# Kernel tuning notes

Hardware: AMD Instinct MI355X
Metric: run time of the kernel (lower is better)

Reference implementation:

```python
import jax, jax.numpy as jnp
import numpy as np

N_FFT = 200; HOP = 100; N_FREQ = N_FFT // 2 + 1  # 101
EMB = 256; HEADS = 8; DHEAD = EMB // HEADS; DEPTH = 4
N_CH = 23; B = 256; TS = 2000
MASK_RATIO = 0.9


def _layernorm(x, s, b):
    mu = jnp.mean(x, -1, keepdims=True)
    var = jnp.mean((x - mu) ** 2, -1, keepdims=True)
    return (x - mu) * jax.lax.rsqrt(var + 1e-5) * s + b


def _posenc(T, d):
    pos = jnp.arange(T, dtype=jnp.float32)[:, None]
    div = jnp.exp(jnp.arange(0, d, 2, dtype=jnp.float32) * (-np.log(10000.0) / d))
    pe = jnp.zeros((T, d), jnp.float32)
    pe = pe.at[:, 0::2].set(jnp.sin(pos * div))
    pe = pe.at[:, 1::2].set(jnp.cos(pos * div))
    return pe


def setup_inputs() -> dict:
    key = jax.random.key(0)
    ks = jax.random.split(key, 12)
    def n(k, shape):
        return (jax.random.normal(k, shape) * 0.02).astype(jnp.float32)
    T = 1 + (TS - N_FFT) // HOP  # 19
    S = N_CH * T                 # 437
    return dict(
        x=jax.random.normal(ks[0], (B, N_CH, TS), jnp.float32),
        mask_noise=jax.random.uniform(ks[1], (B, S, EMB), dtype=jnp.float32),
        W_proj=n(ks[2], (N_FREQ, EMB)), b_proj=jnp.zeros((EMB,), jnp.float32),
        channel_tokens=n(ks[3], (N_CH, EMB)),
        ln1_s=jnp.ones((DEPTH, EMB), jnp.float32), ln1_b=jnp.zeros((DEPTH, EMB), jnp.float32),
        Wq=n(ks[4], (DEPTH, EMB, EMB)), Wk=n(ks[5], (DEPTH, EMB, EMB)),
        Wv=n(ks[6], (DEPTH, EMB, EMB)), Wo=n(ks[7], (DEPTH, EMB, EMB)),
        bo=jnp.zeros((DEPTH, EMB), jnp.float32),
        ln2_s=jnp.ones((DEPTH, EMB), jnp.float32), ln2_b=jnp.zeros((DEPTH, EMB), jnp.float32),
        W1=n(ks[8], (DEPTH, EMB, 4 * EMB)), b1=jnp.zeros((DEPTH, 4 * EMB), jnp.float32),
        W2=n(ks[9], (DEPTH, 4 * EMB, EMB)), b2=jnp.zeros((DEPTH, EMB), jnp.float32),
    )


def _forward(x, mask_noise, W_proj, b_proj, channel_tokens,
             ln1_s, ln1_b, Wq, Wk, Wv, Wo, bo, ln2_s, ln2_b, W1, b1, W2, b2):
    Bb, C, ts = x.shape
    T = 1 + (ts - N_FFT) // HOP
    # ---- vectorized per-channel STFT (rect window, center=False, onesided) ----
    idx = jnp.arange(T)[:, None] * HOP + jnp.arange(N_FFT)[None, :]  # [T, n_fft]
    frames = x[:, :, idx]                                            # [B,C,T,n_fft]
    spec = jnp.abs(jnp.fft.rfft(frames, axis=-1)).astype(x.dtype)    # [B,C,T,F]
    # patch embedding (Linear over freq), channel token, positional encoding
    emb = spec @ W_proj + b_proj                                     # [B,C,T,E]
    emb = emb + channel_tokens[:C][None, :, None, :]
    emb = emb + _posenc(T, emb.shape[-1])[None, None]
    emb = emb.reshape(Bb, C * T, -1)                                 # [B,S,E]
    # ---- random masking (mask_ratio=0.9 as hard-coded in forward) ----
    mask = mask_noise < MASK_RATIO
    masked = jnp.where(mask, jnp.zeros((), emb.dtype), emb)
    # ---- LinearAttentionTransformer (non-causal linear attention, pre-norm) ----
    h = masked
    for l in range(DEPTH):
        y = _layernorm(h, ln1_s[l], ln1_b[l])
        S = y.shape[1]
        q = (y @ Wq[l]).reshape(Bb, S, HEADS, DHEAD).transpose(0, 2, 1, 3)
        k = (y @ Wk[l]).reshape(Bb, S, HEADS, DHEAD).transpose(0, 2, 1, 3)
        v = (y @ Wv[l]).reshape(Bb, S, HEADS, DHEAD).transpose(0, 2, 1, 3)
        q = jax.nn.softmax(q, axis=-1) * (DHEAD ** -0.5)
        k = jax.nn.softmax(k, axis=2)  # softmax over sequence
        ctx = jnp.einsum('bhnd,bhne->bhde', k, v)     # [B,H,d,d] global context
        att = jnp.einsum('bhnd,bhde->bhne', q, ctx)   # [B,H,S,d]
        att = att.transpose(0, 2, 1, 3).reshape(Bb, S, EMB)
        h = h + att @ Wo[l] + bo[l]
        y = _layernorm(h, ln2_s[l], ln2_b[l])
        h = h + jax.nn.gelu(y @ W1[l] + b1[l]) @ W2[l] + b2[l]
    return emb, masked, h, mask


def reference(x, mask_noise, W_proj, b_proj, channel_tokens,
              ln1_s, ln1_b, Wq, Wk, Wv, Wo, bo, ln2_s, ln2_b, W1, b1, W2, b2):
    return _forward(x, mask_noise, W_proj, b_proj, channel_tokens,
                    ln1_s, ln1_b, Wq, Wk, Wv, Wo, bo, ln2_s, ln2_b, W1, b1, W2, b2)
```

## Files before the change

kernel.cpp:

```cpp
#include <hip/hip_runtime.h>

#define BB    256
#define NCH   23
#define TT    19
#define SS    437
#define BSR   111872
#define EMBD  256
#define NHEAD 8
#define DH    32
#define NFREQ 101
#define NFFT  200
#define HOPSZ 100
#define TSLEN 2000
#define HID   1024
#define NDEPTH 4
#define NTOK  28639232
#define QKVW  768
#define WL    786432
#define CDL   3584

typedef __attribute__((ext_vector_type(8))) __bf16 bf16x8;
typedef __attribute__((ext_vector_type(8))) unsigned short u16x8;
typedef __attribute__((ext_vector_type(4))) float  f32x4;

__device__ __forceinline__ float gelu_f(float x){
    return 0.5f*x*(1.0f + tanhf(0.7978845608028654f*(x + 0.044715f*x*x*x)));
}
__device__ __forceinline__ unsigned short f2b(float f){
    unsigned u = __float_as_uint(f);
    return (unsigned short)((u + 0x7FFFu + ((u >> 16) & 1u)) >> 16);
}
__device__ __forceinline__ float b2f(unsigned short h){
    return __uint_as_float(((unsigned)h) << 16);
}

__device__ __forceinline__ void swz_tile(int& bx, int& by){
    int nx = gridDim.x, nwg = nx * gridDim.y;
    int lid = blockIdx.y * nx + blockIdx.x;
    int q = nwg >> 3, r = nwg & 7;
    int xcd = lid & 7, off = lid >> 3;
    int wgid = (xcd < r ? xcd*(q+1) : r*(q+1) + (xcd-r)*q) + off;
    bx = wgid % nx; by = wgid / nx;
}

__global__ void init_twb(unsigned short* __restrict__ tw){
    int i = blockIdx.x*256 + threadIdx.x;
    if(i >= 256*256) return;
    int n = i >> 8, k = i & 255;
    float v = 0.f;
    if(k < NFFT && n < 2*NFREQ){
        int f = n >> 1;
        int ph = (f * k) % NFFT;
        float ang = 6.283185307179586f * (float)ph / (float)NFFT;
        v = (n & 1) ? sinf(ang) : cosf(ang);
    }
    tw[i] = f2b(v);
}

__global__ void init_pe(float* __restrict__ pe){
    int i = blockIdx.x*256 + threadIdx.x;
    if(i >= TT*EMBD) return;
    int t = i / EMBD, e = i % EMBD;
    int j = e >> 1;
    float div = expf((float)(2*j) * (-9.210340371976184f/256.0f));
    float ang = (float)t * div;
    pe[i] = (e & 1) ? cosf(ang) : sinf(ang);
}

__global__ void wprep_proj(const float* __restrict__ Wp, unsigned short* __restrict__ Wt){
    int i = blockIdx.x*256 + threadIdx.x;
    if(i >= 256*128) return;
    int e = i >> 7, k = i & 127;
    Wt[i] = f2b(k < NFREQ ? Wp[(size_t)k*EMBD + e] : 0.f);
}

__global__ void wprep_qkv(const float* __restrict__ Wq, const float* __restrict__ Wk,
                          const float* __restrict__ Wv, const float* __restrict__ ln1s,
                          unsigned short* __restrict__ wbuf){
    long i = (long)blockIdx.x*256 + threadIdx.x;
    if(i >= (long)NDEPTH*QKVW*EMBD) return;
    int l = (int)(i / (QKVW*EMBD));
    int rem = (int)(i % (QKVW*EMBD));
    int n = rem >> 8, k = rem & 255;
    const float* W = (n < 256) ? Wq : (n < 512) ? Wk : Wv;
    float s = ln1s[l*EMBD + k];
    wbuf[(size_t)l*WL + rem] = f2b(s * W[(size_t)l*65536 + (size_t)k*256 + (n & 255)]);
}
__global__ void wprep_wo(const float* __restrict__ Wo, unsigned short* __restrict__ wbuf){
    int i = blockIdx.x*256 + threadIdx.x;
    if(i >= NDEPTH*65536) return;
    int l = i >> 16, rem = i & 65535;
    int n = rem >> 8, k = rem & 255;
    wbuf[(size_t)l*WL + 196608 + rem] = f2b(Wo[(size_t)l*65536 + (size_t)k*256 + n]);
}
__global__ void wprep_w1(const float* __restrict__ W1, const float* __restrict__ ln2s,
                         unsigned short* __restrict__ wbuf){
    long i = (long)blockIdx.x*256 + threadIdx.x;
    if(i >= (long)NDEPTH*262144) return;
    int l = (int)(i >> 18), rem = (int)(i & 262143);
    int n = rem >> 8, k = rem & 255;
    float s = ln2s[l*EMBD + k];
    wbuf[(size_t)l*WL + 262144 + rem] = f2b(s * W1[(size_t)l*262144 + (size_t)k*1024 + n]);
}
__global__ void wprep_w2(const float* __restrict__ W2, unsigned short* __restrict__ wbuf){
    long i = (long)blockIdx.x*256 + threadIdx.x;
    if(i >= (long)NDEPTH*262144) return;
    int l = (int)(i >> 18), rem = (int)(i & 262143);
    int n = rem >> 10, k = rem & 1023;
    wbuf[(size_t)l*WL + 524288 + rem] = f2b(W2[(size_t)l*262144 + (size_t)k*256 + n]);
}

__global__ void prep_cd(const float* __restrict__ Wq, const float* __restrict__ Wk,
                        const float* __restrict__ Wv, const float* __restrict__ W1,
                        const float* __restrict__ ln1s, const float* __restrict__ ln1b,
                        const float* __restrict__ ln2s, const float* __restrict__ ln2b,
                        const float* __restrict__ b1, float* __restrict__ cd){
    int i = blockIdx.x*256 + threadIdx.x;
    if(i >= NDEPTH*1792) return;
    int l = i / 1792, r = i % 1792;
    float c = 0.f, d = 0.f;
    if(r < 768){
        const float* W = (r < 256) ? Wq : (r < 512) ? Wk : Wv;
        int n = r & 255;
        for(int k = 0; k < 256; ++k){
            float w = W[(size_t)l*65536 + (size_t)k*256 + n];
            c = fmaf(ln1s[l*EMBD+k], w, c);
            d = fmaf(ln1b[l*EMBD+k], w, d);
        }
        cd[(size_t)l*CDL + r]       = c;
        cd[(size_t)l*CDL + 768 + r] = d;
    } else {
        int n = r - 768;
        for(int k = 0; k < 256; ++k){
            float w = W1[(size_t)l*262144 + (size_t)k*1024 + n];
            c = fmaf(ln2s[l*EMBD+k], w, c);
            d = fmaf(ln2b[l*EMBD+k], w, d);
        }
        cd[(size_t)l*CDL + 1536 + n] = c;
        cd[(size_t)l*CDL + 2560 + n] = d + b1[l*HID + n];
    }
}

#define GEMM_CORE(A_, B_, K_) \
    f32x4 acc[4][4]; \
    _Pragma("unroll") \
    for(int i=0;i<4;++i) \
        _Pragma("unroll") \
        for(int jj=0;jj<4;++jj) acc[i][jj] = (f32x4){0.f,0.f,0.f,0.f}; \
    const int srow0 = w*32 + (l>>3); \
    const int sgrp  = l & 7; \
    for(int k0 = 0; k0 < (K_); k0 += 64){ \
        _Pragma("unroll") \
        for(int it=0; it<4; ++it){ \
            int row  = srow0 + it*8; \
            int colA = ((sgrp ^ (row & 7)) << 3); \
            const unsigned short* ga = (A_) + (size_t)(m0+row)*(K_) + k0 + colA; \
            const unsigned short* gb = (B_) + (size_t)(n0+row)*(K_) + k0 + colA; \
            __builtin_amdgcn_global_load_lds( \
                (__attribute__((address_space(1))) void*)ga, \
                (__attribute__((address_space(3))) void*)(As + w*2048 + it*512), \
                16, 0, 0); \
            __builtin_amdgcn_global_load_lds( \
                (__attribute__((address_space(1))) void*)gb, \
                (__attribute__((address_space(3))) void*)(Bs + w*2048 + it*512), \
                16, 0, 0); \
        } \
        __syncthreads(); \
        GEMM_MFMA_PHASE \
        __syncthreads(); \
    }

#define GEMM_MFMA_PHASE \
        _Pragma("unroll") \
        for(int kk=0; kk<2; ++kk){ \
            bf16x8 af[4], bfr[4]; \
            _Pragma("unroll") \
            for(int mi=0;mi<4;++mi){ \
                int row = wr*64 + mi*16 + (l & 15); \
                int grp = kk*4 + (l >> 4); \
                af[mi] = *(const bf16x8*)&As[row*64 + ((grp ^ (row&7))<<3)]; \
            } \
            _Pragma("unroll") \
            for(int ni=0;ni<4;++ni){ \
                int row = wc*64 + ni*16 + (l & 15); \
                int grp = kk*4 + (l >> 4); \
                bfr[ni] = *(const bf16x8*)&Bs[row*64 + ((grp ^ (row&7))<<3)]; \
            } \
            _Pragma("unroll") \
            for(int mi=0;mi<4;++mi) \
                _Pragma("unroll") \
                for(int ni=0;ni<4;++ni) \
                    acc[mi][ni] = __builtin_amdgcn_mfma_f32_16x16x32_bf16( \
                        af[mi], bfr[ni], acc[mi][ni], 0, 0, 0); \
        }

#define STATS_REDUCE_STORE(rb_, s1_, s2_) \
    { \
        _Pragma("unroll") \
        for(int o=1;o<16;o<<=1){ s1_ += __shfl_xor(s1_, o, 64); s2_ += __shfl_xor(s2_, o, 64); } \
        if(cn == 0){ \
            slds[((rb_)*2 + wc)*2 + 0] = s1_; \
            slds[((rb_)*2 + wc)*2 + 1] = s2_; \
        } \
    }

template<int MODE, int STATS>
__global__ __launch_bounds__(256, 4) void gemm_mfma(
    const unsigned short* __restrict__ A, const unsigned short* __restrict__ Bt,
    const float* __restrict__ bias, void* __restrict__ Cv,
    const unsigned short* __restrict__ Cin, float* __restrict__ sums,
    int M, int N, int K)
{
    __shared__ __align__(16) unsigned short As[128*64];
    __shared__ __align__(16) unsigned short Bs[128*64];
    const int tid = threadIdx.x;
    const int w = tid >> 6, l = tid & 63;
    int bx, by; swz_tile(bx, by);
    const int m0 = by * 128, n0 = bx * 128;
    const int wr = w >> 1, wc = w & 1;
    GEMM_CORE(A, Bt, K)
    const int cn  = l & 15;
    const int cr4 = (l >> 4) * 4;
    float* slds = (float*)As;
    float bnv[4];
    #pragma unroll
    for(int ni=0;ni<4;++ni) bnv[ni] = bias[n0 + wc*64 + ni*16 + cn];
    #pragma unroll
    for(int mi=0;mi<4;++mi){
        #pragma unroll
        for(int r=0;r<4;++r){
            int rb = wr*64 + mi*16 + cr4 + r;
            int m  = m0 + rb;
            float s1 = 0.f, s2 = 0.f;
            #pragma unroll
            for(int ni=0;ni<4;++ni){
                int n = n0 + wc*64 + ni*16 + cn;
                size_t off = (size_t)m*N + n;
                float v = b2f(Cin[off]) + acc[mi][ni][r] + bnv[ni];
                if(MODE == 1) ((unsigned short*)Cv)[off] = f2b(v);
                else          ((float*)Cv)[off] = v;
                if(STATS){ s1 += v; s2 += v*v; }
            }
            if(STATS) STATS_REDUCE_STORE(rb, s1, s2)
        }
    }
    if(STATS){
        __syncthreads();
        if(tid < 128){
            float t1 = slds[(tid*2+0)*2+0] + slds[(tid*2+1)*2+0];
            float t2 = slds[(tid*2+0)*2+1] + slds[(tid*2+1)*2+1];
            atomicAdd(&sums[(size_t)(m0+tid)*2],   t1);
            atomicAdd(&sums[(size_t)(m0+tid)*2+1], t2);
        }
    }
}

template<int GELU>
__global__ __launch_bounds__(256, 4) void gemm_ln(
    const unsigned short* __restrict__ A, const unsigned short* __restrict__ Bt,
    void* __restrict__ Cv, const float* __restrict__ sums,
    const float* __restrict__ cvec, const float* __restrict__ dvec,
    int M, int N, int K)
{
    __shared__ __align__(16) unsigned short As[128*64];
    __shared__ __align__(16) unsigned short Bs[128*64];
    const int tid = threadIdx.x;
    const int w = tid >> 6, l = tid & 63;
    int bx, by; swz_tile(bx, by);
    const int m0 = by * 128, n0 = bx * 128;
    const int wr = w >> 1, wc = w & 1;
    GEMM_CORE(A, Bt, K)
    const int cn  = l & 15;
    const int cr4 = (l >> 4) * 4;
    float cv[4], dv[4];
    #pragma unroll
    for(int ni=0;ni<4;++ni){
        int n = n0 + wc*64 + ni*16 + cn;
        cv[ni] = cvec[n]; dv[ni] = dvec[n];
    }
    #pragma unroll
    for(int mi=0;mi<4;++mi){
        #pragma unroll
        for(int r=0;r<4;++r){
            int m = m0 + wr*64 + mi*16 + cr4 + r;
            float mu  = sums[(size_t)m*2]   * (1.0f/256.0f);
            float ex2 = sums[(size_t)m*2+1] * (1.0f/256.0f);
            float rs = rsqrtf(ex2 - mu*mu + 1e-5f);
            float c0 = rs * mu;
            #pragma unroll
            for(int ni=0;ni<4;++ni){
                int n = n0 + wc*64 + ni*16 + cn;
                float y = rs*acc[mi][ni][r] - c0*cv[ni] + dv[ni];
                ((unsigned short*)Cv)[(size_t)m*N + n] = f2b(GELU ? gelu_f(y) : y);
            }
        }
    }
}

__global__ __launch_bounds__(256) void gemm_dft(
    const float* __restrict__ x, const unsigned short* __restrict__ Bt,
    unsigned short* __restrict__ spec)
{
    const int K = 256;
    __shared__ __align__(16) unsigned short As[128*64];
    __shared__ __align__(16) unsigned short Bs[128*64];
    const int tid = threadIdx.x;
    const int w = tid >> 6, l = tid & 63;
    int bx, by; swz_tile(bx, by);
    const int m0 = by * 128, n0 = bx * 128;
    const int wr = w >> 1, wc = w & 1;
    f32x4 acc[4][4];
    #pragma unroll
    for(int i=0;i<4;++i)
        #pragma unroll
        for(int jj=0;jj<4;++jj) acc[i][jj] = (f32x4){0.f,0.f,0.f,0.f};
    const int sgrp = l & 7;
    for(int k0 = 0; k0 < K; k0 += 64){
        #pragma unroll
        for(int it=0; it<4; ++it){
            int row = w*32 + it*8 + (l>>3);
            int kg  = sgrp ^ (row & 7);
            int kb  = k0 + kg*8;
            int m   = m0 + row;
            int t   = m % TT;
            long bc = m / TT;
            const float* src = x + bc*(long)TSLEN + (long)t*HOPSZ + kb;
            u16x8 v;
            #pragma unroll
            for(int j=0;j<8;++j){
                float f = (kb + j < NFFT) ? src[j] : 0.f;
                v[j] = f2b(f);
            }
            *(u16x8*)&As[row*64 + sgrp*8] = v;
            int colB = (kg << 3);
            const unsigned short* gb = Bt + (size_t)(n0+row)*K + k0 + colB;
            __builtin_amdgcn_global_load_lds(
                (__attribute__((address_space(1))) void*)gb,
                (__attribute__((address_space(3))) void*)(Bs + w*2048 + it*512),
                16, 0, 0);
        }
        __syncthreads();
        GEMM_MFMA_PHASE
        __syncthreads();
    }
    const int cn  = l & 15;
    const int cr4 = (l >> 4) * 4;
    #pragma unroll
    for(int ni=0;ni<4;++ni){
        int n = n0 + wc*64 + ni*16 + cn;
        #pragma unroll
        for(int mi=0;mi<4;++mi){
            int mB = m0 + wr*64 + mi*16 + cr4;
            #pragma unroll
            for(int r=0;r<4;++r){
                float own = acc[mi][ni][r];
                float par = __shfl_xor(own, 1, 64);
                if(!(cn & 1)){
                    float sv = sqrtf(own*own + par*par);
                    spec[(size_t)(mB+r)*128 + (n >> 1)] = f2b(sv);
                }
            }
        }
    }
}

__global__ __launch_bounds__(256) void gemm_emb(
    const unsigned short* __restrict__ A, const unsigned short* __restrict__ Bt,
    const float* __restrict__ bp, const float* __restrict__ ctok,
    const float* __restrict__ pe, const float* __restrict__ noise,
    float* __restrict__ o_emb, float* __restrict__ o_masked,
    float* __restrict__ o_mask, unsigned short* __restrict__ bufH,
    float* __restrict__ sums)
{
    const int K = 128, N = 256;
    __shared__ __align__(16) unsigned short As[128*64];
    __shared__ __align__(16) unsigned short Bs[128*64];
    const int tid = threadIdx.x;
    const int w = tid >> 6, l = tid & 63;
    int bx, by; swz_tile(bx, by);
    const int m0 = by * 128, n0 = bx * 128;
    const int wr = w >> 1, wc = w & 1;
    GEMM_CORE(A, Bt, K)
    const int cn  = l & 15;
    const int cr4 = (l >> 4) * 4;
    float* slds = (float*)As;
    float bnv[4];
    #pragma unroll
    for(int ni=0;ni<4;++ni) bnv[ni] = bp[n0 + wc*64 + ni*16 + cn];
    #pragma unroll
    for(int mi=0;mi<4;++mi){
        #pragma unroll
        for(int r=0;r<4;++r){
            int rb = wr*64 + mi*16 + cr4 + r;
            int m  = m0 + rb;
            int t = m % TT;
            int c = (m / TT) % NCH;
            float s1 = 0.f, s2 = 0.f;
            #pragma unroll
            for(int ni=0;ni<4;++ni){
                int n = n0 + wc*64 + ni*16 + cn;
                size_t off = (size_t)m*EMBD + n;
                float v = acc[mi][ni][r] + bnv[ni] + ctok[c*EMBD + n] + pe[t*EMBD + n];
                o_emb[off] = v;
                float mn = noise[off];
                bool  msk = mn < 0.9f;
                float md = msk ? 0.f : v;
                bufH[off]     = f2b(md);
                o_masked[off] = md;
                o_mask[off]   = msk ? 1.f : 0.f;
                s1 += md; s2 += md*md;
            }
            STATS_REDUCE_STORE(rb, s1, s2)
        }
    }
    __syncthreads();
    if(tid < 128){
        float t1 = slds[(tid*2+0)*2+0] + slds[(tid*2+1)*2+0];
        float t2 = slds[(tid*2+0)*2+1] + slds[(tid*2+1)*2+1];
        atomicAdd(&sums[(size_t)(m0+tid)*2],   t1);
        atomicAdd(&sums[(size_t)(m0+tid)*2+1], t2);
    }
}

__global__ __launch_bounds__(256) void ctx_kernel(const unsigned short* __restrict__ qkvb,
    float* __restrict__ ctx)
{
    __shared__ float kt[16][DH], vt[16][DH];
    __shared__ float sm[8][32], ss[8][32];
    __shared__ float kmsL[32], kinvL[32];
    int bh = blockIdx.x; int b = bh >> 3, h = bh & 7;
    int tid = threadIdx.x;
    {
        int d = tid & 31, g = tid >> 5;
        const unsigned short* p = qkvb + (size_t)b*SS*QKVW + 256 + h*DH + d;
        float m = -1e30f, s = 0.f;
        for(int n = g; n < SS; n += 8){
            float xv = b2f(p[(size_t)n*QKVW]);
            if(xv > m){ s = s*expf(m-xv) + 1.f; m = xv; }
            else      { s += expf(xv-m); }
        }
        sm[g][d] = m; ss[g][d] = s;
    }
    __syncthreads();
    if(tid < 32){
        float M = sm[0][tid], S = ss[0][tid];
        #pragma unroll
        for(int o = 1; o < 8; ++o){
            float m2 = sm[o][tid], s2 = ss[o][tid];
            if(m2 > M){ S = S*expf(M-m2) + s2; M = m2; }
            else      { S += s2*expf(m2-M); }
        }
        kmsL[tid] = M; kinvL[tid] = 1.0f / S;
    }
    __syncthreads();
    int d = tid >> 3, e4 = (tid & 7) * 4;
    float km = kmsL[d];
    float a0=0,a1=0,a2=0,a3=0;
    for(int n0=0;n0<SS;n0+=16){
        __syncthreads();
        #pragma unroll
        for(int i=0;i<2;++i){
            int e = tid + i*256;
            int nn = e >> 5, dd = e & 31;
            int n = n0 + nn;
            float kv, vv;
            if(n < SS){
                size_t off = ((size_t)(b*SS+n))*QKVW + h*DH + dd;
                kv = b2f(qkvb[off + 256]);
                vv = b2f(qkvb[off + 512]);
            } else { kv = -1e30f; vv = 0.f; }
            kt[nn][dd] = kv; vt[nn][dd] = vv;
        }
        __syncthreads();
        #pragma unroll
        for(int nn=0;nn<16;++nn){
            float ke = expf(kt[nn][d] - km);
            a0 = fmaf(ke, vt[nn][e4+0], a0);
            a1 = fmaf(ke, vt[nn][e4+1], a1);
            a2 = fmaf(ke, vt[nn][e4+2], a2);
            a3 = fmaf(ke, vt[nn][e4+3], a3);
        }
    }
    float inv = kinvL[d];
    float* op = ctx + ((size_t)bh*DH + d)*DH + e4;
    op[0]=a0*inv; op[1]=a1*inv; op[2]=a2*inv; op[3]=a3*inv;
}

__global__ __launch_bounds__(256) void att_kernel(const unsigned short* __restrict__ qkvb,
    const float* __restrict__ ctx, unsigned short* __restrict__ att)
{
    __shared__ float qs[4][EMBD];
    int w = threadIdx.x >> 6, lane = threadIdx.x & 63;
    int b = blockIdx.y;
    int s = blockIdx.x*4 + w;
    if(s >= SS) return;
    long row = (long)b*SS + s;
    ushort4 qu = *(const ushort4*)(qkvb + (size_t)row*QKVW + lane*4);
    float4 q4 = make_float4(b2f(qu.x), b2f(qu.y), b2f(qu.z), b2f(qu.w));
    float m = fmaxf(fmaxf(q4.x,q4.y), fmaxf(q4.z,q4.w));
    #pragma unroll
    for(int o=1;o<8;o<<=1) m = fmaxf(m, __shfl_xor(m, o, 64));
    float e0 = expf(q4.x-m), e1 = expf(q4.y-m), e2 = expf(q4.z-m), e3 = expf(q4.w-m);
    float ssum = e0+e1+e2+e3;
    #pragma unroll
    for(int o=1;o<8;o<<=1) ssum += __shfl_xor(ssum, o, 64);
    float sc = 0.17677669529663687f / ssum;
    *(float4*)&qs[w][lane*4] = make_float4(e0*sc, e1*sc, e2*sc, e3*sc);
    int head = lane >> 3;
    int ecol = (lane & 7) * 4;
    const float* cb = ctx + ((size_t)(b*NHEAD + head))*DH*DH + ecol;
    float a0=0,a1=0,a2=0,a3=0;
    #pragma unroll
    for(int d=0; d<DH; ++d){
        float qd = qs[w][head*DH + d];
        float4 c4 = *(const float4*)(cb + d*DH);
        a0 = fmaf(qd, c4.x, a0);
        a1 = fmaf(qd, c4.y, a1);
        a2 = fmaf(qd, c4.z, a2);
        a3 = fmaf(qd, c4.w, a3);
    }
    ushort4 o4; o4.x=f2b(a0); o4.y=f2b(a1); o4.z=f2b(a2); o4.w=f2b(a3);
    *(ushort4*)(att + row*EMBD + lane*4) = o4;
}

extern "C" void kernel_launch(void* const* d_in, const int* in_sizes, int n_in,
                              void* d_out, int out_size, void* d_ws, size_t ws_size,
                              hipStream_t stream)
{
    if(n_in != 18) return;

    const float* x     = (const float*)d_in[0];
    const float* noise = (const float*)d_in[1];
    const float* Wproj = (const float*)d_in[2];
    const float* bproj = (const float*)d_in[3];
    const float* ctok  = (const float*)d_in[4];
    const float* ln1s  = (const float*)d_in[5];
    const float* ln1b  = (const float*)d_in[6];
    const float* Wq    = (const float*)d_in[7];
    const float* Wk    = (const float*)d_in[8];
    const float* Wv    = (const float*)d_in[9];
    const float* Wo    = (const float*)d_in[10];
    const float* bo    = (const float*)d_in[11];
    const float* ln2s  = (const float*)d_in[12];
    const float* ln2b  = (const float*)d_in[13];
    const float* W1    = (const float*)d_in[14];
    const float* b1    = (const float*)d_in[15];
    const float* W2    = (const float*)d_in[16];
    const float* b2    = (const float*)d_in[17];

    char* p = (char*)d_ws;
    unsigned short* bufHb = (unsigned short*)p;           p += (size_t)NTOK*2;
    float* big = (float*)p;                               p += (size_t)NTOK*2*4;
    unsigned short* qkvb   = (unsigned short*)big;
    unsigned short* hidb   = (unsigned short*)big;
    unsigned short* specb  = (unsigned short*)p;          p += (size_t)BSR*128*2;
    unsigned short* attb   = (unsigned short*)p;          p += (size_t)NTOK*2;
    float* sums1 = (float*)p;                             p += (size_t)BSR*2*4;
    float* sums2 = (float*)p;                             p += (size_t)BSR*2*4;
    float* cdb  = (float*)p;                              p += (size_t)NDEPTH*CDL*4;
    float* ctxb = (float*)p;                              p += (size_t)BB*NHEAD*DH*DH*4;
    float* peb  = (float*)p;                              p += (size_t)TT*EMBD*4;
    unsigned short* twb  = (unsigned short*)p;            p += (size_t)65536*2;
    unsigned short* Wpb  = (unsigned short*)p;            p += (size_t)32768*2;
    unsigned short* wbuf = (unsigned short*)p;            p += (size_t)4*WL*2;
    if(ws_size < (size_t)(p - (char*)d_ws)) return;

    float* out      = (float*)d_out;
    float* o_emb    = out;
    float* o_masked = out + (size_t)NTOK;
    float* o_h      = out + 2*(size_t)NTOK;
    float* o_mask   = out + 3*(size_t)NTOK;

    dim3 blk(256);
    const size_t SB = (size_t)BSR*2*4;

    init_twb<<<256, blk, 0, stream>>>(twb);
    init_pe <<<19,  blk, 0, stream>>>(peb);
    wprep_proj<<<128, blk, 0, stream>>>(Wproj, Wpb);
    wprep_qkv<<<3072, blk, 0, stream>>>(Wq, Wk, Wv, ln1s, wbuf);
    wprep_wo <<<1024, blk, 0, stream>>>(Wo, wbuf);
    wprep_w1 <<<4096, blk, 0, stream>>>(W1, ln2s, wbuf);
    wprep_w2 <<<4096, blk, 0, stream>>>(W2, wbuf);
    prep_cd  <<<28,   blk, 0, stream>>>(Wq, Wk, Wv, W1, ln1s, ln1b, ln2s, ln2b, b1, cdb);

    hipMemsetAsync(sums1, 0, SB, stream);
    gemm_dft<<<dim3(2,874), blk, 0, stream>>>(x, twb, specb);
    gemm_emb<<<dim3(2,874), blk, 0, stream>>>(specb, Wpb, bproj, ctok, peb, noise,
                                              o_emb, o_masked, o_mask, bufHb, sums1);

    for(int l=0;l<NDEPTH;++l){
        unsigned short* wl   = wbuf + (size_t)l*WL;
        unsigned short* Wqkv = wl;
        unsigned short* Wot  = wl + 196608;
        unsigned short* W1t  = wl + 262144;
        unsigned short* W2t  = wl + 524288;
        float* cq = cdb + (size_t)l*CDL;
        float* dq = cq + 768;
        float* c1 = cq + 1536;
        float* d1 = cq + 2560;

        gemm_ln<0><<<dim3(6,874), blk, 0, stream>>>(bufHb, Wqkv, qkvb,
                                    sums1, cq, dq, BSR, QKVW, EMBD);
        ctx_kernel<<<BB*NHEAD, blk, 0, stream>>>(qkvb, ctxb);
        att_kernel<<<dim3(110, BB), blk, 0, stream>>>(qkvb, ctxb, attb);
        hipMemsetAsync(sums2, 0, SB, stream);
        gemm_mfma<1,1><<<dim3(2,874), blk, 0, stream>>>(attb, Wot, bo + l*EMBD, bufHb,
                                    bufHb, sums2, BSR, EMBD, EMBD);
        gemm_ln<1><<<dim3(8,874), blk, 0, stream>>>(bufHb, W1t, hidb,
                                    sums2, c1, d1, BSR, HID, EMBD);
        if(l == NDEPTH-1){
            gemm_mfma<4,0><<<dim3(2,874), blk, 0, stream>>>(hidb, W2t, b2 + l*EMBD, o_h,
                                    bufHb, nullptr, BSR, EMBD, HID);
        } else {
            hipMemsetAsync(sums1, 0, SB, stream);
            gemm_mfma<1,1><<<dim3(2,874), blk, 0, stream>>>(hidb, W2t, b2 + l*EMBD, bufHb,
                                    bufHb, sums1, BSR, EMBD, HID);
        }
    }
}
```

Before: 2.961 ms.

## Use 256x256 tiles with double-buffered LDS pipeline for transformer GEMMs

```diff
diff --git a/kernel.cpp b/kernel.cpp
--- a/kernel.cpp
+++ b/kernel.cpp
@@ -23,6 +23,9 @@
 typedef __attribute__((ext_vector_type(8))) unsigned short u16x8;
 typedef __attribute__((ext_vector_type(4))) float  f32x4;
 
+#define AS1 __attribute__((address_space(1)))
+#define AS3 __attribute__((address_space(3)))
+
 __device__ __forceinline__ float gelu_f(float x){
     return 0.5f*x*(1.0f + tanhf(0.7978845608028654f*(x + 0.044715f*x*x*x)));
 }
@@ -157,79 +160,107 @@
             const unsigned short* ga = (A_) + (size_t)(m0+row)*(K_) + k0 + colA; \
             const unsigned short* gb = (B_) + (size_t)(n0+row)*(K_) + k0 + colA; \
             __builtin_amdgcn_global_load_lds( \
-                (__attribute__((address_space(1))) void*)ga, \
-                (__attribute__((address_space(3))) void*)(As + w*2048 + it*512), \
-                16, 0, 0); \
+                (AS1 void*)ga, (AS3 void*)(As + w*2048 + it*512), 16, 0, 0); \
             __builtin_amdgcn_global_load_lds( \
-                (__attribute__((address_space(1))) void*)gb, \
-                (__attribute__((address_space(3))) void*)(Bs + w*2048 + it*512), \
-                16, 0, 0); \
+                (AS1 void*)gb, (AS3 void*)(Bs + w*2048 + it*512), 16, 0, 0); \
         } \
         __syncthreads(); \
-        GEMM_MFMA_PHASE \
+        GEMM_MFMA_PHASE(As, Bs, 4, wr*64, wc*64) \
         __syncthreads(); \
     }
 
-#define GEMM_MFMA_PHASE \
+#define GEMM_MFMA_PHASE(Ab_, Bb_, MREP_, MBASE_, NBASE_) \
         _Pragma("unroll") \
         for(int kk=0; kk<2; ++kk){ \
-            bf16x8 af[4], bfr[4]; \
+            bf16x8 af[MREP_], bq[4]; \
             _Pragma("unroll") \
-            for(int mi=0;mi<4;++mi){ \
-                int row = wr*64 + mi*16 + (l & 15); \
+            for(int mi=0;mi<(MREP_);++mi){ \
+                int row = (MBASE_) + mi*16 + (l & 15); \
                 int grp = kk*4 + (l >> 4); \
-                af[mi] = *(const bf16x8*)&As[row*64 + ((grp ^ (row&7))<<3)]; \
+                af[mi] = *(const bf16x8*)&(Ab_)[row*64 + ((grp ^ (row&7))<<3)]; \
             } \
             _Pragma("unroll") \
             for(int ni=0;ni<4;++ni){ \
-                int row = wc*64 + ni*16 + (l & 15); \
+                int row = (NBASE_) + ni*16 + (l & 15); \
                 int grp = kk*4 + (l >> 4); \
-                bfr[ni] = *(const bf16x8*)&Bs[row*64 + ((grp ^ (row&7))<<3)]; \
+                bq[ni] = *(const bf16x8*)&(Bb_)[row*64 + ((grp ^ (row&7))<<3)]; \
             } \
             _Pragma("unroll") \
-            for(int mi=0;mi<4;++mi) \
+            for(int mi=0;mi<(MREP_);++mi) \
                 _Pragma("unroll") \
                 for(int ni=0;ni<4;++ni) \
                     acc[mi][ni] = __builtin_amdgcn_mfma_f32_16x16x32_bf16( \
-                        af[mi], bfr[ni], acc[mi][ni], 0, 0, 0); \
-        }
-
-#define STATS_REDUCE_STORE(rb_, s1_, s2_) \
-    { \
-        _Pragma("unroll") \
-        for(int o=1;o<16;o<<=1){ s1_ += __shfl_xor(s1_, o, 64); s2_ += __shfl_xor(s2_, o, 64); } \
-        if(cn == 0){ \
-            slds[((rb_)*2 + wc)*2 + 0] = s1_; \
-            slds[((rb_)*2 + wc)*2 + 1] = s2_; \
+                        af[mi], bq[ni], acc[mi][ni], 0, 0, 0); \
+        }
+
+#define STAGE256(Ad_, Bd_, A_, B_, K_, kt_) \
+    { int k0s = (kt_) << 6; \
+      _Pragma("unroll") \
+      for(int it=0; it<4; ++it){ \
+        int row = srow + it*64; \
+        int colA = ((sgrp ^ (row & 7)) << 3); \
+        __builtin_amdgcn_global_load_lds( \
+            (AS1 void*)((A_) + (size_t)(m0+row)*(K_) + k0s + colA), \
+            (AS3 void*)((Ad_) + it*4096 + w*512), 16, 0, 0); \
+        __builtin_amdgcn_global_load_lds( \
+            (AS1 void*)((B_) + (size_t)(n0+row)*(K_) + k0s + colA), \
+            (AS3 void*)((Bd_) + it*4096 + w*512), 16, 0, 0); \
+      } }
+
+#define KLOOP256(A_, B_, K_) \
+    const int nt = (K_) >> 6; \
+    STAGE256(&As2[0][0], &Bs2[0][0], A_, B_, K_, 0) \
+    for(int t = 0; t < nt; ++t){ \
+        unsigned short* Ac = &As2[t & 1][0]; \
+        unsigned short* Bc = &Bs2[t & 1][0]; \
+        if(t + 1 < nt){ \
+            STAGE256(&As2[(t+1)&1][0], &Bs2[(t+1)&1][0], A_, B_, K_, t+1) \
+            asm volatile("s_waitcnt vmcnt(8)" ::: "memory"); \
+            __builtin_amdgcn_sched_barrier(0); \
+            __builtin_amdgcn_s_barrier(); \
+            __builtin_amdgcn_sched_barrier(0); \
+        } else { \
+            __syncthreads(); \
         } \
+        __builtin_amdgcn_s_setprio(1); \
+        GEMM_MFMA_PHASE(Ac, Bc, 8, wr*128, wc*64) \
+        __builtin_amdgcn_s_setprio(0); \
+        __builtin_amdgcn_sched_barrier(0); \
+        __builtin_amdgcn_s_barrier(); \
+        __builtin_amdgcn_sched_barrier(0); \
     }
 
 template<int MODE, int STATS>
-__global__ __launch_bounds__(256, 4) void gemm_mfma(
+__global__ __launch_bounds__(512, 2) void gemm_mfma256(
     const unsigned short* __restrict__ A, const unsigned short* __restrict__ Bt,
     const float* __restrict__ bias, void* __restrict__ Cv,
     const unsigned short* __restrict__ Cin, float* __restrict__ sums,
     int M, int N, int K)
 {
-    __shared__ __align__(16) unsigned short As[128*64];
-    __shared__ __align__(16) unsigned short Bs[128*64];
+    __shared__ __align__(16) unsigned short As2[2][16384];
+    __shared__ __align__(16) unsigned short Bs2[2][16384];
     const int tid = threadIdx.x;
     const int w = tid >> 6, l = tid & 63;
     int bx, by; swz_tile(bx, by);
-    const int m0 = by * 128, n0 = bx * 128;
-    const int wr = w >> 1, wc = w & 1;
-    GEMM_CORE(A, Bt, K)
-    const int cn  = l & 15;
-    const int cr4 = (l >> 4) * 4;
-    float* slds = (float*)As;
+    const int m0 = by * 256, n0 = bx * 256;
+    const int wr = w >> 2, wc = w & 3;
+    const int srow = tid >> 3, sgrp = tid & 7;
+    f32x4 acc[8][4];
+    #pragma unroll
+    for(int i=0;i<8;++i)
+        #pragma unroll
+        for(int j=0;j<4;++j) acc[i][j] = (f32x4){0.f,0.f,0.f,0.f};
+    KLOOP256(A, Bt, K)
+    const int cn = l & 15, cr4 = (l >> 4) * 4;
+    float* slds = (float*)&As2[0][0];
     float bnv[4];
     #pragma unroll
     for(int ni=0;ni<4;++ni) bnv[ni] = bias[n0 + wc*64 + ni*16 + cn];
     #pragma unroll
-    for(int mi=0;mi<4;++mi){
+    for(int mi=0;mi<8;++mi){
         #pragma unroll
         for(int r=0;r<4;++r){
-            int rb = wr*64 + mi*16 + cr4 + r;
+            int rb = wr*128 + mi*16 + cr4 + r;
             int m  = m0 + rb;
             float s1 = 0.f, s2 = 0.f;
             #pragma unroll
@@ -241,14 +272,22 @@
                 else          ((float*)Cv)[off] = v;
                 if(STATS){ s1 += v; s2 += v*v; }
             }
-            if(STATS) STATS_REDUCE_STORE(rb, s1, s2)
+            if(STATS){
+                #pragma unroll
+                for(int o=1;o<16;o<<=1){ s1 += __shfl_xor(s1,o,64); s2 += __shfl_xor(s2,o,64); }
+                if(cn == 0){
+                    slds[(rb*4 + wc)*2 + 0] = s1;
+                    slds[(rb*4 + wc)*2 + 1] = s2;
+                }
+            }
         }
     }
     if(STATS){
         __syncthreads();
-        if(tid < 128){
-            float t1 = slds[(tid*2+0)*2+0] + slds[(tid*2+1)*2+0];
-            float t2 = slds[(tid*2+0)*2+1] + slds[(tid*2+1)*2+1];
+        if(tid < 256){
+            float t1 = 0.f, t2 = 0.f;
+            #pragma unroll
+            for(int q=0;q<4;++q){ t1 += slds[(tid*4+q)*2]; t2 += slds[(tid*4+q)*2+1]; }
             atomicAdd(&sums[(size_t)(m0+tid)*2],   t1);
             atomicAdd(&sums[(size_t)(m0+tid)*2+1], t2);
         }
@@ -256,33 +295,38 @@
 }
 
 template<int GELU>
-__global__ __launch_bounds__(256, 4) void gemm_ln(
+__global__ __launch_bounds__(512, 2) void gemm_ln256(
     const unsigned short* __restrict__ A, const unsigned short* __restrict__ Bt,
     void* __restrict__ Cv, const float* __restrict__ sums,
     const float* __restrict__ cvec, const float* __restrict__ dvec,
     int M, int N, int K)
 {
-    __shared__ __align__(16) unsigned short As[128*64];
-    __shared__ __align__(16) unsigned short Bs[128*64];
+    __shared__ __align__(16) unsigned short As2[2][16384];
+    __shared__ __align__(16) unsigned short Bs2[2][16384];
     const int tid = threadIdx.x;
     const int w = tid >> 6, l = tid & 63;
     int bx, by; swz_tile(bx, by);
-    const int m0 = by * 128, n0 = bx * 128;
-    const int wr = w >> 1, wc = w & 1;
-    GEMM_CORE(A, Bt, K)
-    const int cn  = l & 15;
-    const int cr4 = (l >> 4) * 4;
-    float cv[4], dv[4];
+    const int m0 = by * 256, n0 = bx * 256;
+    const int wr = w >> 2, wc = w & 3;
+    const int srow = tid >> 3, sgrp = tid & 7;
+    f32x4 acc[8][4];
+    #pragma unroll
+    for(int i=0;i<8;++i)
+        #pragma unroll
+        for(int j=0;j<4;++j) acc[i][j] = (f32x4){0.f,0.f,0.f,0.f};
+    KLOOP256(A, Bt, K)
+    const int cn = l & 15, cr4 = (l >> 4) * 4;
+    float cv4[4], dv4[4];
     #pragma unroll
     for(int ni=0;ni<4;++ni){
         int n = n0 + wc*64 + ni*16 + cn;
-        cv[ni] = cvec[n]; dv[ni] = dvec[n];
-    }
-    #pragma unroll
-    for(int mi=0;mi<4;++mi){
+        cv4[ni] = cvec[n]; dv4[ni] = dvec[n];
+    }
+    #pragma unroll
+    for(int mi=0;mi<8;++mi){
         #pragma unroll
         for(int r=0;r<4;++r){
-            int m = m0 + wr*64 + mi*16 + cr4 + r;
+            int m = m0 + wr*128 + mi*16 + cr4 + r;
             float mu  = sums[(size_t)m*2]   * (1.0f/256.0f);
             float ex2 = sums[(size_t)m*2+1] * (1.0f/256.0f);
             float rs = rsqrtf(ex2 - mu*mu + 1e-5f);
@@ -290,7 +334,7 @@
             #pragma unroll
             for(int ni=0;ni<4;++ni){
                 int n = n0 + wc*64 + ni*16 + cn;
-                float y = rs*acc[mi][ni][r] - c0*cv[ni] + dv[ni];
+                float y = rs*acc[mi][ni][r] - c0*cv4[ni] + dv4[ni];
                 ((unsigned short*)Cv)[(size_t)m*N + n] = f2b(GELU ? gelu_f(y) : y);
             }
         }
@@ -335,12 +379,10 @@
             int colB = (kg << 3);
             const unsigned short* gb = Bt + (size_t)(n0+row)*K + k0 + colB;
             __builtin_amdgcn_global_load_lds(
-                (__attribute__((address_space(1))) void*)gb,
-                (__attribute__((address_space(3))) void*)(Bs + w*2048 + it*512),
-                16, 0, 0);
+                (AS1 void*)gb, (AS3 void*)(Bs + w*2048 + it*512), 16, 0, 0);
         }
         __syncthreads();
-        GEMM_MFMA_PHASE
+        GEMM_MFMA_PHASE(As, Bs, 4, wr*64, wc*64)
         __syncthreads();
     }
     const int cn  = l & 15;
@@ -410,7 +452,12 @@
                 o_mask[off]   = msk ? 1.f : 0.f;
                 s1 += md; s2 += md*md;
             }
-            STATS_REDUCE_STORE(rb, s1, s2)
+            #pragma unroll
+            for(int o=1;o<16;o<<=1){ s1 += __shfl_xor(s1,o,64); s2 += __shfl_xor(s2,o,64); }
+            if(cn == 0){
+                slds[(rb*2 + wc)*2 + 0] = s1;
+                slds[(rb*2 + wc)*2 + 1] = s2;
+            }
         }
     }
     __syncthreads();
@@ -572,6 +619,7 @@
     float* o_mask   = out + 3*(size_t)NTOK;
 
     dim3 blk(256);
+    dim3 blk5(512);
     const size_t SB = (size_t)BSR*2*4;
 
     init_twb<<<256, blk, 0, stream>>>(twb);
@@ -599,22 +647,22 @@
         float* c1 = cq + 1536;
         float* d1 = cq + 2560;
 
-        gemm_ln<0><<<dim3(6,874), blk, 0, stream>>>(bufHb, Wqkv, qkvb,
+        gemm_ln256<0><<<dim3(3,437), blk5, 0, stream>>>(bufHb, Wqkv, qkvb,
                                     sums1, cq, dq, BSR, QKVW, EMBD);
         ctx_kernel<<<BB*NHEAD, blk, 0, stream>>>(qkvb, ctxb);
         att_kernel<<<dim3(110, BB), blk, 0, stream>>>(qkvb, ctxb, attb);
         hipMemsetAsync(sums2, 0, SB, stream);
-        gemm_mfma<1,1><<<dim3(2,874), blk, 0, stream>>>(attb, Wot, bo + l*EMBD, bufHb,
-                                    bufHb, sums2, BSR, EMBD, EMBD);
-        gemm_ln<1><<<dim3(8,874), blk, 0, stream>>>(bufHb, W1t, hidb,
+        gemm_mfma256<1,1><<<dim3(1,437), blk5, 0, stream>>>(attb, Wot, bo + l*EMBD,
+                                    bufHb, bufHb, sums2, BSR, EMBD, EMBD);
+        gemm_ln256<1><<<dim3(4,437), blk5, 0, stream>>>(bufHb, W1t, hidb,
                                     sums2, c1, d1, BSR, HID, EMBD);
         if(l == NDEPTH-1){
-            gemm_mfma<4,0><<<dim3(2,874), blk, 0, stream>>>(hidb, W2t, b2 + l*EMBD, o_h,
-                                    bufHb, nullptr, BSR, EMBD, HID);
+            gemm_mfma256<4,0><<<dim3(1,437), blk5, 0, stream>>>(hidb, W2t, b2 + l*EMBD,
+                                    o_h, bufHb, nullptr, BSR, EMBD, HID);
         } else {
             hipMemsetAsync(sums1, 0, SB, stream);
-            gemm_mfma<1,1><<<dim3(2,874), blk, 0, stream>>>(hidb, W2t, b2 + l*EMBD, bufHb,
-                                    bufHb, sums1, BSR, EMBD, HID);
-        }
-    }
-}
+            gemm_mfma256<1,1><<<dim3(1,437), blk5, 0, stream>>>(hidb, W2t, b2 + l*EMBD,
+                                    bufHb, bufHb, sums1, BSR, EMBD, HID);
+        }
+    }
+}
```

Result: slower. 3.358 ms (+13.4%).
